# Kernel optimization log

Measured on AMD Instinct MI355X. Metric: run time of the kernel, lower is better.

The kernel has to match this reference:

```python
import jax, jax.numpy as jnp
import numpy as np

N_HOPS = 3
VOCAB, D = 100000, 300
B, S, T = 128, 2048, 4
N_CLASSES = 3


def setup_inputs() -> dict:
    key = jax.random.key(0)
    ks = jax.random.split(key, 9)
    return {
        "inputs": jax.random.randint(ks[0], (B, S), 0, VOCAB, dtype=jnp.int64 if jax.config.jax_enable_x64 else jnp.int32),
        "targets": jax.random.randint(ks[1], (B, T), 0, VOCAB, dtype=jnp.int64 if jax.config.jax_enable_x64 else jnp.int32),
        "emb_table": jax.random.normal(ks[2], (VOCAB, D), dtype=jnp.float32) * 0.1,
        "W_att": jax.random.normal(ks[3], (2 * D, 1), dtype=jnp.float32) * 0.05,
        "b_att": jax.random.normal(ks[4], (1,), dtype=jnp.float32) * 0.05,
        "W_tr": jax.random.normal(ks[5], (D, D), dtype=jnp.float32) * 0.05,
        "b_tr": jax.random.normal(ks[6], (D,), dtype=jnp.float32) * 0.05,
        "W_out": jax.random.normal(ks[7], (D, N_CLASSES), dtype=jnp.float32) * 0.05,
        "b_out": jax.random.normal(ks[8], (N_CLASSES,), dtype=jnp.float32) * 0.05,
    }


def reference(inputs, targets, emb_table, W_att, b_att, W_tr, b_tr, W_out, b_out):
    # Embedding lookups (dropout prob = 0.0 -> identity)
    we = emb_table[inputs]    # [B, S, D] word/context embeddings
    te = emb_table[targets]   # [B, T, D] aspect-term embeddings
    d = we.shape[-1]
    # Split concat-linear: cat([we, u]) @ W_att == we @ Wa + u @ Wu (avoids [B,S,2D] intermediate)
    Wa, Wu = W_att[:d], W_att[d:]          # each [D, 1]
    u = jnp.mean(te, axis=1, keepdims=True)  # [B, 1, D]
    for _ in range(N_HOPS):
        g = jnp.tanh(we @ Wa + u @ Wu + b_att)          # [B, S, 1]
        a = jax.nn.softmax(g, axis=1)                    # softmax over sequence
        vec = jnp.einsum('bs,bsd->bd', a[..., 0], we)    # [B, D] attention-weighted sum
        te = vec[:, None, :] + te @ W_tr + b_tr          # [B, T, D] (broadcast add)
        u = jnp.mean(te, axis=1, keepdims=True)          # [B, 1, D]
    return u[:, 0, :] @ W_out + b_out                    # [B, n_classes]
```

## Files before the change

### kernel.cpp

```cpp
#include <hip/hip_runtime.h>
#include <hip/hip_bf16.h>

#define VOCAB 100000
#define D 300
#define B 128
#define S 2048
#define T 4

#define WS_V      0
#define WS_WTWU   3600
#define WS_WT2WU  3900
#define WS_WTWO   4200
#define WS_W2WO   5100
#define WS_WT3WO  6000
#define WS_CONST  6900
#define WS_PROJ   7940


__device__ __forceinline__ float wave_red(float x) {
    #pragma unroll
    for (int m = 1; m < 64; m <<= 1) x += __shfl_xor(x, m, 64);
    return x;
}

__device__ __forceinline__ float fast_tanh(float x) {
    float e = __expf(2.0f * x);
    return 1.0f - 2.0f / (e + 1.0f);
}

__global__ __launch_bounds__(64) void k_derive1(const float* __restrict__ Watt,
                                                const float* __restrict__ Wtr,
                                                const float* __restrict__ Wout,
                                                float* __restrict__ ws) {
    int i = blockIdx.x, lane = threadIdx.x;
    const float* wrow = Wtr + (size_t)i * D;
    float au = 0.f, a0 = 0.f, a1 = 0.f, a2 = 0.f;
    for (int j = lane; j < D; j += 64) {
        float w = wrow[j];
        au += w * Watt[D + j];
        a0 += w * Wout[j * 3 + 0];
        a1 += w * Wout[j * 3 + 1];
        a2 += w * Wout[j * 3 + 2];
    }
    au = wave_red(au); a0 = wave_red(a0); a1 = wave_red(a1); a2 = wave_red(a2);
    if (lane == 0) {
        ws[WS_WTWU + i] = au;
        ws[WS_WTWO + i * 3 + 0] = a0;
        ws[WS_WTWO + i * 3 + 1] = a1;
        ws[WS_WTWO + i * 3 + 2] = a2;
    }
}

__global__ __launch_bounds__(64) void k_derive2(const float* __restrict__ Watt,
                                                const float* __restrict__ Wtr,
                                                const float* __restrict__ Wout,
                                                float* __restrict__ ws) {
    int i = blockIdx.x, lane = threadIdx.x;
    const float* wrow = Wtr + (size_t)i * D;
    float au = 0.f, a0 = 0.f, a1 = 0.f, a2 = 0.f;
    for (int j = lane; j < D; j += 64) {
        float w = wrow[j];
        au += w * ws[WS_WTWU + j];
        a0 += w * ws[WS_WTWO + j * 3 + 0];
        a1 += w * ws[WS_WTWO + j * 3 + 1];
        a2 += w * ws[WS_WTWO + j * 3 + 2];
    }
    au = wave_red(au); a0 = wave_red(a0); a1 = wave_red(a1); a2 = wave_red(a2);
    if (lane == 0) {
        ws[WS_WT2WU + i] = au;
        ws[WS_W2WO + i * 3 + 0] = a0;
        ws[WS_W2WO + i * 3 + 1] = a1;
        ws[WS_W2WO + i * 3 + 2] = a2;
    }
    if (lane < 12) {
        float val;
        if      (lane == 0)  val = Watt[i];
        else if (lane == 1)  val = Watt[D + i];
        else if (lane == 2)  val = ws[WS_WTWU + i];
        else if (lane < 6)   val = Wout[i * 3 + (lane - 3)];
        else if (lane < 9)   val = ws[WS_WTWO + i * 3 + (lane - 6)];
        else if (lane == 9)  val = a0;
        else if (lane == 10) val = a1;
        else                 val = a2;
        ws[WS_V + i * 12 + lane] = val;
    }
}

__global__ __launch_bounds__(64) void k_derive3(const float* __restrict__ Watt,
                                                const float* __restrict__ Wtr,
                                                const float* __restrict__ Wout,
                                                const float* __restrict__ btr,
                                                float* __restrict__ ws) {
    int lane = threadIdx.x;
    if (blockIdx.x < D) {
        int i = blockIdx.x;
        const float* wrow = Wtr + (size_t)i * D;
        float a0 = 0.f, a1 = 0.f, a2 = 0.f;
        for (int j = lane; j < D; j += 64) {
            float w = wrow[j];
            a0 += w * ws[WS_W2WO + j * 3 + 0];
            a1 += w * ws[WS_W2WO + j * 3 + 1];
            a2 += w * ws[WS_W2WO + j * 3 + 2];
        }
        a0 = wave_red(a0); a1 = wave_red(a1); a2 = wave_red(a2);
        if (lane == 0) {
            ws[WS_WT3WO + i * 3 + 0] = a0;
            ws[WS_WT3WO + i * 3 + 1] = a1;
            ws[WS_WT3WO + i * 3 + 2] = a2;
        }
    } else {
        float acc[11];
        #pragma unroll
        for (int k = 0; k < 11; ++k) acc[k] = 0.f;
        for (int i = lane; i < D; i += 64) {
            float bt = btr[i];
            acc[0]  += bt * Watt[D + i];
            acc[1]  += bt * ws[WS_WTWU + i];
            acc[2]  += bt * Wout[i * 3 + 0];
            acc[3]  += bt * Wout[i * 3 + 1];
            acc[4]  += bt * Wout[i * 3 + 2];
            acc[5]  += bt * ws[WS_WTWO + i * 3 + 0];
            acc[6]  += bt * ws[WS_WTWO + i * 3 + 1];
            acc[7]  += bt * ws[WS_WTWO + i * 3 + 2];
            acc[8]  += bt * ws[WS_W2WO + i * 3 + 0];
            acc[9]  += bt * ws[WS_W2WO + i * 3 + 1];
            acc[10] += bt * ws[WS_W2WO + i * 3 + 2];
        }
        #pragma unroll
        for (int k = 0; k < 11; ++k) acc[k] = wave_red(acc[k]);
        if (lane == 0) {
            #pragma unroll
            for (int k = 0; k < 11; ++k) ws[WS_CONST + k] = acc[k];
        }
    }
}

__global__ __launch_bounds__(256) void k_proj(const float* __restrict__ E,
                                              const float* __restrict__ Vg,
                                              float* __restrict__ proj) {
    __shared__ float4 sbuf[256 * 16];
    const int tid   = threadIdx.x;
    const int R0    = blockIdx.x * 256;
    const int myrow = R0 + tid;
    const float4* E4 = (const float4*)E;

    float acc[12];
    #pragma unroll
    for (int c = 0; c < 12; ++c) acc[c] = 0.f;

    for (int ch = 0; ch < 5; ++ch) {
        #pragma unroll
        for (int j = 0; j < 15; ++j) {
            int L = tid + j * 256;
            int r = L / 15;
            int m = L - r * 15;
            float4 v = make_float4(0.f, 0.f, 0.f, 0.f);
            int gr = R0 + r;
            if (gr < VOCAB) v = E4[(size_t)gr * 75 + ch * 15 + m];
            sbuf[r * 16 + (m ^ (r & 15))] = v;
        }
        __syncthreads();
        if (myrow < VOCAB) {
            #pragma unroll
            for (int m = 0; m < 15; ++m) {
                float4 e = sbuf[tid * 16 + (m ^ (tid & 15))];
                const float* vp = Vg + (ch * 60 + m * 4) * 12;
                #pragma unroll
                for (int c = 0; c < 12; ++c) {
                    acc[c] += e.x * vp[c]      + e.y * vp[12 + c]
                            + e.z * vp[24 + c] + e.w * vp[36 + c];
                }
            }
        }
        __syncthreads();
    }

    if (myrow < VOCAB) {
        float4* dst = (float4*)(proj + (size_t)myrow * 12);
        dst[0] = make_float4(acc[0], acc[1], acc[2],  acc[3]);
        dst[1] = make_float4(acc[4], acc[5], acc[6],  acc[7]);
        dst[2] = make_float4(acc[8], acc[9], acc[10], acc[11]);
    }
}

__global__ __launch_bounds__(1024) void k_hops(const int* __restrict__ inputs,
                                               const int* __restrict__ targets,
                                               const float* __restrict__ E,
                                               const float* __restrict__ Watt,
                                               const float* __restrict__ ws,
                                               const float* __restrict__ batt,
                                               const float* __restrict__ bout,
                                               float* __restrict__ out) {
    __shared__ float wred[16][13];
    __shared__ float Ash[13];
    __shared__ float dsc[8];
    __shared__ float sc[4];
    int b = blockIdx.x, tid = threadIdx.x, wave = tid >> 6, lane = tid & 63;
    const float* proj = ws + WS_PROJ;
    const float* cst  = ws + WS_CONST;
    const int*   inp  = inputs + (size_t)b * S;

    float pv[2][12];
    #pragma unroll
    for (int q = 0; q < 2; ++q) {
        int s = tid + 1024 * q;
        int idx = inp[s];
        const float4* pr = (const float4*)(proj + (size_t)idx * 12);
        float4 x = pr[0], y = pr[1], z = pr[2];
        pv[q][0] = x.x; pv[q][1] = x.y; pv[q][2]  = x.z; pv[q][3]  = x.w;
        pv[q][4] = y.x; pv[q][5] = y.y; pv[q][6]  = y.z; pv[q][7]  = y.w;
        pv[q][8] = z.x; pv[q][9] = z.y; pv[q][10] = z.z; pv[q][11] = z.w;
    }

    if (wave < 6) {
        const int* tg = targets + b * T;
        const float* r0 = E + (size_t)tg[0] * D;
        const float* r1 = E + (size_t)tg[1] * D;
        const float* r2 = E + (size_t)tg[2] * D;
        const float* r3 = E + (size_t)tg[3] * D;
        float s = 0.f;
        for (int i = lane; i < D; i += 64) {
            float u = 0.25f * (r0[i] + r1[i] + r2[i] + r3[i]);
            float v;
            if      (wave == 0) v = Watt[D + i];
            else if (wave == 1) v = ws[WS_WTWU + i];
            else if (wave == 2) v = ws[WS_WT2WU + i];
            else if (wave == 3) v = ws[WS_WT3WO + i * 3 + 0];
            else if (wave == 4) v = ws[WS_WT3WO + i * 3 + 1];
            else                v = ws[WS_WT3WO + i * 3 + 2];
            s += u * v;
        }
        s = wave_red(s);
        if (lane == 0) dsc[wave] = s;
    }
    __syncthreads();
    float c = dsc[0] + batt[0];

    float o3c0 = 0.f, o3c1 = 0.f, o3c2 = 0.f, uWtWu = 0.f;

    #pragma unroll
    for (int hop = 0; hop < 3; ++hop) {
        float acc[12];
        #pragma unroll
        for (int k = 0; k < 12; ++k) acc[k] = 0.f;
        #pragma unroll
        for (int q = 0; q < 2; ++q) {
            float g = fast_tanh(pv[q][0] + c);
            float e = __expf(g);
            acc[11] += e;
            #pragma unroll
            for (int k = 1; k < 12; ++k) acc[k - 1] += e * pv[q][k];
        }
        #pragma unroll
        for (int m = 1; m < 64; m <<= 1) {
            #pragma unroll
            for (int k = 0; k < 12; ++k) acc[k] += __shfl_xor(acc[k], m, 64);
        }
        if (lane == 0) {
            #pragma unroll
            for (int k = 0; k < 12; ++k) wred[wave][k] = acc[k];
        }
        __syncthreads();
        if (tid < 12) {
            float s = 0.f;
            #pragma unroll
            for (int w = 0; w < 16; ++w) s += wred[w][tid];
            Ash[tid] = s;
        }
        __syncthreads();
        if (tid == 0) {
            float inv = 1.0f / Ash[11];
            if (hop == 0) {
                o3c0  = Ash[8] * inv + dsc[3] + cst[8];
                o3c1  = Ash[9] * inv + dsc[4] + cst[9];
                o3c2  = Ash[10] * inv + dsc[5] + cst[10];
                uWtWu = Ash[1] * inv + dsc[2] + cst[1];
                sc[0] = Ash[0] * inv + dsc[1] + cst[0] + batt[0];
            } else if (hop == 1) {
                o3c0  = Ash[5] * inv + o3c0 + cst[5];
                o3c1  = Ash[6] * inv + o3c1 + cst[6];
                o3c2  = Ash[7] * inv + o3c2 + cst[7];
                sc[0] = Ash[0] * inv + uWtWu + cst[0] + batt[0];
            } else {
                out[b * 3 + 0] = Ash[2] * inv + o3c0 + cst[2] + bout[0];
                out[b * 3 + 1] = Ash[3] * inv + o3c1 + cst[3] + bout[1];
                out[b * 3 + 2] = Ash[4] * inv + o3c2 + cst[4] + bout[2];
            }
        }
        __syncthreads();
        c = sc[0];
    }
}

extern "C" void kernel_launch(void* const* d_in, const int* in_sizes, int n_in,
                              void* d_out, int out_size, void* d_ws, size_t ws_size,
                              hipStream_t stream) {
    const int*   inputs  = (const int*)  d_in[0];
    const int*   targets = (const int*)  d_in[1];
    const float* emb     = (const float*)d_in[2];
    const float* Watt    = (const float*)d_in[3];
    const float* batt    = (const float*)d_in[4];
    const float* Wtr     = (const float*)d_in[5];
    const float* btr     = (const float*)d_in[6];
    const float* Wout    = (const float*)d_in[7];
    const float* bout    = (const float*)d_in[8];
    float* ws  = (float*)d_ws;
    float* out = (float*)d_out;

    hipLaunchKernelGGL(k_derive1, dim3(D),     dim3(64),   0, stream, Watt, Wtr, Wout, ws);
    hipLaunchKernelGGL(k_derive2, dim3(D),     dim3(64),   0, stream, Watt, Wtr, Wout, ws);
    hipLaunchKernelGGL(k_derive3, dim3(D + 1), dim3(64),   0, stream, Watt, Wtr, Wout, btr, ws);
    hipLaunchKernelGGL(k_proj,    dim3(391),   dim3(256),  0, stream, emb, ws + WS_V, ws + WS_PROJ);
    hipLaunchKernelGGL(k_hops,    dim3(B),     dim3(1024), 0, stream, inputs, targets, emb, Watt,
                       ws, batt, bout, out);
}
```

Before: 255.7 us.

## Split projection rows across five waves with shared-memory reduction instead of LDS staging

The vocabulary projection kernel now assigns 64 rows per block and splits each row's 300-wide dot products across five waves (one 60-element chunk each). Each wave reads its chunk directly from global memory, and partial sums are combined through a small shared-memory reduction. This drops the staged, swizzled LDS tile and its per-chunk barriers and launches four times as many blocks for better latency hiding. The cost is that each lane reads uncoalesced strided float4s straight from global memory (a 1200-byte row stride across lanes), plus an extra reduction step.

Result: slower. 387.7 us (+51.6%).

```diff
diff --git a/kernel.cpp b/kernel.cpp
--- a/kernel.cpp
+++ b/kernel.cpp
@@ -135,48 +135,44 @@
     }
 }
 
-__global__ __launch_bounds__(256) void k_proj(const float* __restrict__ E,
-                                              const float* __restrict__ Vg,
-                                              float* __restrict__ proj) {
-    __shared__ float4 sbuf[256 * 16];
-    const int tid   = threadIdx.x;
-    const int R0    = blockIdx.x * 256;
-    const int myrow = R0 + tid;
-    const float4* E4 = (const float4*)E;
+__global__ __launch_bounds__(320, 8) void k_proj(const float* __restrict__ E,
+                                                 const float* __restrict__ Vg,
+                                                 float* __restrict__ proj) {
+    __shared__ float red[5][64][13];
+    const int tid  = threadIdx.x;
+    const int w    = tid >> 6;
+    const int lane = tid & 63;
+    const int row  = blockIdx.x * 64 + lane;
+    const bool valid = row < VOCAB;
 
     float acc[12];
     #pragma unroll
     for (int c = 0; c < 12; ++c) acc[c] = 0.f;
 
-    for (int ch = 0; ch < 5; ++ch) {
-        #pragma unroll
-        for (int j = 0; j < 15; ++j) {
-            int L = tid + j * 256;
-            int r = L / 15;
-            int m = L - r * 15;
-            float4 v = make_float4(0.f, 0.f, 0.f, 0.f);
-            int gr = R0 + r;
-            if (gr < VOCAB) v = E4[(size_t)gr * 75 + ch * 15 + m];
-            sbuf[r * 16 + (m ^ (r & 15))] = v;
-        }
-        __syncthreads();
-        if (myrow < VOCAB) {
-            #pragma unroll
-            for (int m = 0; m < 15; ++m) {
-                float4 e = sbuf[tid * 16 + (m ^ (tid & 15))];
-                const float* vp = Vg + (ch * 60 + m * 4) * 12;
-                #pragma unroll
-                for (int c = 0; c < 12; ++c) {
-                    acc[c] += e.x * vp[c]      + e.y * vp[12 + c]
-                            + e.z * vp[24 + c] + e.w * vp[36 + c];
-                }
+    if (valid) {
+        const float4* er = (const float4*)(E + (size_t)row * D) + w * 15;
+        #pragma unroll 5
+        for (int m = 0; m < 15; ++m) {
+            float4 e = er[m];
+            const float* vp = Vg + (w * 15 + m) * 48;
+            #pragma unroll
+            for (int c = 0; c < 12; ++c) {
+                acc[c] += e.x * vp[c]      + e.y * vp[12 + c]
+                        + e.z * vp[24 + c] + e.w * vp[36 + c];
             }
         }
-        __syncthreads();
-    }
-
-    if (myrow < VOCAB) {
-        float4* dst = (float4*)(proj + (size_t)myrow * 12);
+    }
+
+    #pragma unroll
+    for (int c = 0; c < 12; ++c) red[w][lane][c] = acc[c];
+    __syncthreads();
+
+    if (w == 0 && valid) {
+        #pragma unroll
+        for (int ww = 1; ww < 5; ++ww)
+            #pragma unroll
+            for (int c = 0; c < 12; ++c) acc[c] += red[ww][lane][c];
+        float4* dst = (float4*)(proj + (size_t)row * 12);
         dst[0] = make_float4(acc[0], acc[1], acc[2],  acc[3]);
         dst[1] = make_float4(acc[4], acc[5], acc[6],  acc[7]);
         dst[2] = make_float4(acc[8], acc[9], acc[10], acc[11]);
@@ -310,7 +306,7 @@
     hipLaunchKernelGGL(k_derive1, dim3(D),     dim3(64),   0, stream, Watt, Wtr, Wout, ws);
     hipLaunchKernelGGL(k_derive2, dim3(D),     dim3(64),   0, stream, Watt, Wtr, Wout, ws);
     hipLaunchKernelGGL(k_derive3, dim3(D + 1), dim3(64),   0, stream, Watt, Wtr, Wout, btr, ws);
-    hipLaunchKernelGGL(k_proj,    dim3(391),   dim3(256),  0, stream, emb, ws + WS_V, ws + WS_PROJ);
+    hipLaunchKernelGGL(k_proj,    dim3(1563),  dim3(320),  0, stream, emb, ws + WS_V, ws + WS_PROJ);
     hipLaunchKernelGGL(k_hops,    dim3(B),     dim3(1024), 0, stream, inputs, targets, emb, Watt,
                        ws, batt, bout, out);
 }
```
